# Optimization experiments

Measured on AMD Instinct MI355X. Metric: run time of the kernel, lower is better.

The kernel has to match this reference:

```python
import jax, jax.numpy as jnp
from jax import lax
import numpy as np

B, N_WAY, K_SHOT, Q, IMG = 8, 5, 1, 15, 84
D = 3      # repnet spatial output for imgsz=84
CF = 64    # repnet channels
C2 = CF + 2

def _conv(x, w, b):
    y = lax.conv_general_dilated(x, w, (1, 1), 'VALID', dimension_numbers=('NCHW', 'OIHW', 'NCHW'))
    return y + b[None, :, None, None]

def _maxpool2(x):
    return lax.reduce_window(x, -jnp.inf, lax.max, (1, 1, 2, 2), (1, 1, 2, 2), 'VALID')

def _avgpool5(x):
    return lax.reduce_window(x, 0.0, lax.add, (1, 1, 5, 5), (1, 1, 5, 5), 'VALID') / 25.0

def _bn(x, g, b):
    # train-mode BatchNorm2d: batch statistics over (N, H, W), biased variance, eps=1e-5
    m = jnp.mean(x, (0, 2, 3), keepdims=True)
    v = jnp.var(x, (0, 2, 3), keepdims=True)
    return (x - m) * lax.rsqrt(v + 1e-5) * g[None, :, None, None] + b[None, :, None, None]

def _repnet(x, cw1, cb1, bg1, bb1, cw2, cb2, bg2, bb2, cw3, cb3, bg3, bb3, cw4, cb4, bg4, bb4):
    x = jax.nn.relu(_bn(_maxpool2(_conv(x, cw1, cb1)), bg1, bb1))
    x = jax.nn.relu(_bn(_maxpool2(_conv(x, cw2, cb2)), bg2, bb2))
    x = jax.nn.relu(_bn(_conv(x, cw3, cb3), bg3, bb3))
    x = jax.nn.relu(_bn(_conv(x, cw4, cb4), bg4, bb4))
    return _avgpool5(x)

def _forward(support_x, support_y, query_x, query_y, cw1, cb1, bg1, bb1, cw2, cb2, bg2, bb2, cw3, cb3, bg3, bb3, cw4, cb4, bg4, bb4, gW1, gb1, gW2, gb2, gW3, gb3, gW4, gb4, fW1, fb1, fW2, fb2, fW3, fb3, fW4, fb4):
    b, setsz = support_x.shape[:2]
    q = query_x.shape[1]
    rep = lambda z: _repnet(z, cw1, cb1, bg1, bb1, cw2, cb2, bg2, bb2, cw3, cb3, bg3, bb3, cw4, cb4, bg4, bb4)
    sup = rep(support_x.reshape(b * setsz, 3, IMG, IMG)).reshape(b, setsz, CF, D, D)
    qry = rep(query_x.reshape(b * q, 3, IMG, IMG)).reshape(b, q, CF, D, D)
    sup = sup.reshape(b, N_WAY, K_SHOT, CF, D, D).sum(2)  # sum over shots -> (b, n_way, c, d, d)
    setsz = N_WAY
    sy = support_y[:, ::K_SHOT]
    ii, jj = jnp.meshgrid(jnp.arange(D), jnp.arange(D), indexing='ij')
    coord = jnp.stack([ii, jj]).astype(jnp.float32) / D  # (2, d, d): ch0 = i/d, ch1 = j/d
    sup = jnp.concatenate([sup, jnp.broadcast_to(coord, (b, setsz, 2, D, D))], axis=2)  # (b,s,66,d,d)
    qry = jnp.concatenate([qry, jnp.broadcast_to(coord, (b, q, 2, D, D))], axis=2)      # (b,q,66,d,d)
    d2 = D * D
    sup = sup.reshape(b, setsz, C2, d2)
    qry = qry.reshape(b, q, C2, d2)
    # pair feature is cat([support_feat, query_feat]); split g's first layer so the
    # (b,q,s,d2,d2,2c) pair tensor is never materialized: g1([s;q]) = s@Ws + q@Wq + b1
    Ws, Wq = gW1[:C2], gW1[C2:]
    A = jnp.einsum('bscp,ck->bspk', sup, Ws)   # (b, s, d2, 256)
    Bq = jnp.einsum('bqcp,ck->bqpk', qry, Wq)  # (b, q, d2, 256)
    h = jax.nn.relu(A[:, None, :, :, None, :] + Bq[:, :, None, None, :, :] + gb1)  # (b,q,s,d2,d2,256)
    h = jax.nn.relu(h @ gW2 + gb2)
    h = jax.nn.relu(h @ gW3 + gb3)
    h = jax.nn.relu(h @ gW4 + gb4)
    x_f = h.sum((3, 4))  # sum over all d2*d2 pixel pairs -> (b, q, s, 256)
    h = jax.nn.relu(x_f @ fW1 + fb1)
    h = jax.nn.relu(h @ fW2 + fb2)  # nn.Dropout treated as identity (deterministic reference)
    h = jax.nn.relu(h @ fW3 + fb3)
    o = h @ fW4 + fb4  # (b, q, s, 64)
    score = jnp.sqrt(jnp.sum(o * o, axis=-1))  # L2 norm over feature dim -> (b, q, s)
    n = jnp.sqrt(jnp.sum(score * score, axis=2, keepdims=True))
    score = score / n * (n * n / (1.0 + n * n))  # squash
    ap = sy[:, None, :] == query_y[:, :, None]  # exactly one True per (b, q)
    an = ~ap
    score_ap = jnp.sum(jnp.where(ap, score, 0.0), axis=2, keepdims=True)
    MARGIN = 0.2
    loss = jnp.sum(jax.nn.relu(score - score_ap + MARGIN) * an)
    return loss

def setup_inputs() -> dict:
    key = jax.random.key(0)
    ks = iter(jax.random.split(key, 48))
    nrm = lambda shape, s: jax.random.normal(next(ks), shape, jnp.float32) * s
    inp = {}
    inp['support_x'] = nrm((B, N_WAY * K_SHOT, 3, IMG, IMG), 1.0)
    inp['support_y'] = jnp.tile(jnp.arange(N_WAY, dtype=jnp.int32), (B, 1))
    inp['query_x'] = nrm((B, Q, 3, IMG, IMG), 1.0)
    inp['query_y'] = jax.random.randint(next(ks), (B, Q), 0, N_WAY, dtype=jnp.int32)
    inp['cw1'] = nrm((64, 3, 3, 3), 0.19); inp['cb1'] = nrm((64,), 0.02)
    inp['bg1'] = 1.0 + nrm((64,), 0.05); inp['bb1'] = nrm((64,), 0.02)
    inp['cw2'] = nrm((64, 64, 3, 3), 0.042); inp['cb2'] = nrm((64,), 0.02)
    inp['bg2'] = 1.0 + nrm((64,), 0.05); inp['bb2'] = nrm((64,), 0.02)
    inp['cw3'] = nrm((64, 64, 3, 3), 0.042); inp['cb3'] = nrm((64,), 0.02)
    inp['bg3'] = 1.0 + nrm((64,), 0.05); inp['bb3'] = nrm((64,), 0.02)
    inp['cw4'] = nrm((64, 64, 3, 3), 0.042); inp['cb4'] = nrm((64,), 0.02)
    inp['bg4'] = 1.0 + nrm((64,), 0.05); inp['bb4'] = nrm((64,), 0.02)
    inp['gW1'] = nrm((2 * C2, 256), 0.087); inp['gb1'] = nrm((256,), 0.02)
    inp['gW2'] = nrm((256, 256), 0.0625); inp['gb2'] = nrm((256,), 0.02)
    inp['gW3'] = nrm((256, 256), 0.0625); inp['gb3'] = nrm((256,), 0.02)
    inp['gW4'] = nrm((256, 256), 0.0625); inp['gb4'] = nrm((256,), 0.02)
    inp['fW1'] = nrm((256, 256), 0.0625); inp['fb1'] = nrm((256,), 0.02)
    inp['fW2'] = nrm((256, 256), 0.0625); inp['fb2'] = nrm((256,), 0.02)
    inp['fW3'] = nrm((256, 128), 0.0625); inp['fb3'] = nrm((128,), 0.02)
    inp['fW4'] = nrm((128, 64), 0.088); inp['fb4'] = nrm((64,), 0.02)
    return inp

def reference(support_x, support_y, query_x, query_y, cw1, cb1, bg1, bb1, cw2, cb2, bg2, bb2, cw3, cb3, bg3, bb3, cw4, cb4, bg4, bb4, gW1, gb1, gW2, gb2, gW3, gb3, gW4, gb4, fW1, fb1, fW2, fb2, fW3, fb3, fW4, fb4):
    return _forward(support_x, support_y, query_x, query_y, cw1, cb1, bg1, bb1, cw2, cb2, bg2, bb2, cw3, cb3, bg3, bb3, cw4, cb4, bg4, bb4, gW1, gb1, gW2, gb2, gW3, gb3, gW4, gb4, fW1, fb1, fW2, fb2, fW3, fb3, fW4, fb4)
```

## Files before the change

### kernel.cpp

```cpp
#include <hip/hip_runtime.h>
#include <hip/hip_bf16.h>

typedef __hip_bfloat16 bf16;
typedef __attribute__((ext_vector_type(8))) short short8;
typedef __attribute__((ext_vector_type(4))) short bfx4;
typedef __attribute__((ext_vector_type(4))) float f32x4;

#define DEV __device__ __forceinline__

static constexpr int NSUP = 40;
static constexpr int NQRY = 120;
static constexpr int NIMG = 160;
static constexpr int GM   = 48600;
static constexpr int GMP  = 48640;
static constexpr int NBS  = 128;
static constexpr int NBQ  = 384;

DEV float b2f(short s) {
    union { unsigned int u; float f; } v; v.u = ((unsigned int)(unsigned short)s) << 16; return v.f;
}
DEV short bfbits(float v) {
    bf16 h = __float2bfloat16(v);
    union { bf16 b; short s; } u; u.b = h; return u.s;
}

#define GLL(gp, lp) __builtin_amdgcn_global_load_lds( \
    (const __attribute__((address_space(1))) void*)(gp), \
    (__attribute__((address_space(3))) void*)(lp), 16, 0, 0)

__global__ void nhwc4_kernel(const float* sx, const float* qx, bf16* img) {
    int idx = blockIdx.x * 256 + threadIdx.x;
    if (idx >= NIMG * 7056) return;
    int n = idx / 7056, p = idx % 7056;
    const float* im = ((n < NSUP) ? sx + (size_t)n * 3 * 7056 : qx + (size_t)(n - NSUP) * 3 * 7056) + p;
    bfx4 o;
    o[0] = bfbits(im[0]);
    o[1] = bfbits(im[7056]);
    o[2] = bfbits(im[14112]);
    o[3] = 0;
    *(bfx4*)&img[(size_t)idx * 4] = o;
}

__global__ void wc1m_kernel(const float* cw1, bf16* Wc1) {
    int idx = blockIdx.x * 256 + threadIdx.x;
    if (idx >= 4096) return;
    int oc = idx >> 6, k = idx & 63;
    int ky = k >> 4, r = k & 15;
    float v = 0.f;
    if (ky < 3 && r < 12) {
        int kx = r >> 2, ic = r & 3;
        if (ic < 3) v = cw1[oc * 27 + ic * 9 + ky * 3 + kx];
    }
    Wc1[idx] = __float2bfloat16(v);
}

__global__ __launch_bounds__(256) void conv1m_kernel(
        const bf16* __restrict__ img, const bf16* __restrict__ Wc1,
        const float* __restrict__ cb1, bf16* __restrict__ out) {
    int n = blockIdx.x;
    int wv = threadIdx.x >> 6, ln = threadIdx.x & 63;
    int pr = ln & 15, kg = ln >> 4;
    int t0 = (blockIdx.y * 4 + wv) * 16;
    int t = t0 + pr;
    int tc = t < 1681 ? t : 1680;
    int pyt = tc / 41, pxt = tc % 41;
    const bf16* ib = img + (size_t)n * 28224;

    short8 wf[4][2];
    #pragma unroll
    for (int mt = 0; mt < 4; ++mt)
        #pragma unroll
        for (int h = 0; h < 2; ++h)
            wf[mt][h] = *(const short8*)&Wc1[(size_t)(mt * 16 + pr) * 64 + h * 32 + kg * 8];

    int r8 = (kg & 1) * 8;
    int kyb = kg >> 1;
    short8 pf[4][2];
    #pragma unroll
    for (int nt = 0; nt < 4; ++nt) {
        int py = 2 * pyt + (nt >> 1), px = 2 * pxt + (nt & 1);
        #pragma unroll
        for (int h = 0; h < 2; ++h) {
            int ky = h * 2 + kyb;
            short8 f = {0, 0, 0, 0, 0, 0, 0, 0};
            if (ky < 3) {
                const bf16* p = ib + ((py + ky) * 84 + px) * 4 + r8;
                if (r8 == 0) {
                    bfx4 a0 = *(const bfx4*)p, a1 = *(const bfx4*)(p + 4);
                    f[0] = a0[0]; f[1] = a0[1]; f[2] = a0[2]; f[3] = a0[3];
                    f[4] = a1[0]; f[5] = a1[1]; f[6] = a1[2]; f[7] = a1[3];
                } else {
                    bfx4 a0 = *(const bfx4*)p;
                    f[0] = a0[0]; f[1] = a0[1]; f[2] = a0[2]; f[3] = a0[3];
                }
            }
            pf[nt][h] = f;
        }
    }

    f32x4 acc[4][4];
    #pragma unroll
    for (int a = 0; a < 4; ++a)
        #pragma unroll
        for (int b = 0; b < 4; ++b)
            #pragma unroll
            for (int r = 0; r < 4; ++r) acc[a][b][r] = 0.f;

    #pragma unroll
    for (int h = 0; h < 2; ++h)
        #pragma unroll
        for (int mt = 0; mt < 4; ++mt)
            #pragma unroll
            for (int nt = 0; nt < 4; ++nt)
                acc[mt][nt] = __builtin_amdgcn_mfma_f32_16x16x32_bf16(
                    wf[mt][h], pf[nt][h], acc[mt][nt], 0, 0, 0);

    if (t < 1681) {
        bf16* ob = out + ((size_t)n * 1681 + t) * 64;
        #pragma unroll
        for (int mt = 0; mt < 4; ++mt) {
            f32x4 v = acc[mt][0];
            #pragma unroll
            for (int nt = 1; nt < 4; ++nt)
                #pragma unroll
                for (int r = 0; r < 4; ++r) v[r] = fmaxf(v[r], acc[mt][nt][r]);
            bfx4 o;
            #pragma unroll
            for (int r = 0; r < 4; ++r) o[r] = bfbits(v[r] + cb1[mt * 16 + kg * 4 + r]);
            *(bfx4*)&ob[mt * 16 + kg * 4] = o;
        }
    }
}

__global__ void wtp_kernel(const float* cw2, const float* cw3, const float* cw4, bf16* Wp) {
    int idx = blockIdx.x * 256 + threadIdx.x;
    if (idx >= 3 * 64 * 584) return;
    int L = idx / (64 * 584), r = idx % (64 * 584);
    int oc = r / 584, kk = r % 584;
    const float* src = (L == 0) ? cw2 : (L == 1) ? cw3 : cw4;
    float v = 0.f;
    if (kk < 576) {
        int ic = kk & 63, tap = kk >> 6;
        v = src[oc * 576 + ic * 9 + tap];
    }
    Wp[idx] = __float2bfloat16(v);
}

__global__ void wtg_kernel(const float* gW2, const float* gW3, const float* gW4, bf16* WTg) {
    int idx = blockIdx.x * 256 + threadIdx.x;
    if (idx >= 3 * 65536) return;
    int L = idx >> 16, r = idx & 65535, n = r >> 8, k = r & 255;
    const float* W = (L == 0) ? gW2 : (L == 1) ? gW3 : gW4;
    WTg[idx] = __float2bfloat16(W[k * 256 + n]);
}

__global__ void stats_nhwc_kernel(const bf16* buf, int HW, float* partial) {
    int blk = blockIdx.x;
    bool qg = blk >= NBS;
    int b0 = qg ? blk - NBS : blk;
    int nb = qg ? NBQ : NBS;
    const bf16* base = buf + (qg ? (size_t)NSUP * HW * 64 : 0);
    long rows = (long)(qg ? NQRY : NSUP) * HW;
    int tid = threadIdx.x;
    int sub = tid & 7, rl = tid >> 3;
    float s1[8], s2[8];
    #pragma unroll
    for (int j = 0; j < 8; ++j) { s1[j] = 0.f; s2[j] = 0.f; }
    for (long r = (long)b0 * 32 + rl; r < rows; r += (long)nb * 32) {
        short8 v = *(const short8*)&base[r * 64 + sub * 8];
        #pragma unroll
        for (int j = 0; j < 8; ++j) { float f = b2f(v[j]); s1[j] += f; s2[j] += f * f; }
    }
    __shared__ float l1[256][8], l2[256][8];
    #pragma unroll
    for (int j = 0; j < 8; ++j) { l1[tid][j] = s1[j]; l2[tid][j] = s2[j]; }
    __syncthreads();
    if (tid < 64) {
        int su = tid >> 3, j = tid & 7;
        float a = 0.f, b = 0.f;
        for (int k = 0; k < 32; ++k) { a += l1[su + k * 8][j]; b += l2[su + k * 8][j]; }
        partial[blk * 128 + tid] = a;
        partial[blk * 128 + 64 + tid] = b;
    }
}

__global__ __launch_bounds__(1024) void bnfin_kernel(
        const float* partial, const float* gam, const float* bet,
        int HW, float* scsh) {
    int tid = threadIdx.x;
    int out = tid >> 3;
    int part = tid & 7;
    int g = out >> 6, c = out & 63;
    int b0 = g ? NBS : 0, nb = g ? NBQ : NBS;
    float s1 = 0.f, s2 = 0.f;
    for (int b = b0 + part; b < b0 + nb; b += 8) {
        s1 += partial[b * 128 + c];
        s2 += partial[b * 128 + 64 + c];
    }
    __shared__ float r1[1024], r2[1024];
    r1[tid] = s1; r2[tid] = s2;
    __syncthreads();
    if (part == 0) {
        #pragma unroll
        for (int j = 1; j < 8; ++j) { s1 += r1[tid + j]; s2 += r2[tid + j]; }
        float cnt = (float)((g ? NQRY : NSUP)) * (float)HW;
        float mean = s1 / cnt;
        float var = s2 / cnt - mean * mean;
        float istd = rsqrtf(var + 1e-5f);
        float sc = gam[c] * istd;
        scsh[out] = sc;
        scsh[128 + out] = bet[c] - mean * sc;
    }
}

__global__ void bnrelu_nhwc_kernel(bf16* buf, const float* scsh, int HW, int total8) {
    int idx = blockIdx.x * 256 + threadIdx.x;
    if (idx >= total8) return;
    size_t e0 = (size_t)idx * 8;
    int c0 = (int)(e0 & 63);
    int g = (int)(e0 / ((size_t)HW * 64)) >= NSUP ? 1 : 0;
    short8 v = *(short8*)&buf[e0];
    short8 o;
    #pragma unroll
    for (int j = 0; j < 8; ++j) {
        int c = c0 + j;
        float f = b2f(v[j]) * scsh[g * 64 + c] + scsh[128 + g * 64 + c];
        o[j] = bfbits(fmaxf(f, 0.f));
    }
    *(short8*)&buf[e0] = o;
}

template <int IW, int OW, bool POOL, int NT>
__global__ __launch_bounds__(256) void convmfma_kernel(
        const bf16* __restrict__ in, const bf16* __restrict__ Wp,
        const float* __restrict__ cb, bf16* __restrict__ out) {
    constexpr int M  = OW * OW;
    constexpr int PW = OW / 2;
    constexpr int MP = POOL ? PW * PW : M;
    constexpr int T  = NIMG * MP;
    constexpr int NPF = POOL ? 4 : NT;

    int wv = threadIdx.x >> 6, ln = threadIdx.x & 63;
    int pr = ln & 15, kg = ln >> 4;

    const bf16* pptr[NPF];
    int pxv[NPF];
    if (POOL) {
        int gp = (blockIdx.x * 4 + wv) * 16 + pr;
        int gpc = gp < T ? gp : T - 1;
        pxv[0] = gp;
        int n = gpc / MP, pp = gpc % MP;
        int py = pp / PW, px = pp % PW;
        const bf16* ib = in + (size_t)n * (IW * IW * 64) + kg * 8;
        #pragma unroll
        for (int nt = 0; nt < 4; ++nt)
            pptr[nt] = ib + ((2 * py + (nt >> 1)) * IW + 2 * px + (nt & 1)) * 64;
    } else {
        #pragma unroll
        for (int nt = 0; nt < NT; ++nt) {
            int gp = (blockIdx.x * 4 + wv) * (16 * NT) + nt * 16 + pr;
            int gpc = gp < T ? gp : T - 1;
            pxv[nt] = gp;
            int n = gpc / M, pix = gpc % M;
            int y = pix / OW, x = pix % OW;
            pptr[nt] = in + ((size_t)n * (IW * IW) + y * IW + x) * 64 + kg * 8;
        }
    }
    const bf16* wb = Wp + kg * 8;

    f32x4 acc[4][NPF];
    #pragma unroll
    for (int a = 0; a < 4; ++a)
        #pragma unroll
        for (int b = 0; b < NPF; ++b)
            #pragma unroll
            for (int r = 0; r < 4; ++r) acc[a][b][r] = 0.f;

    #pragma unroll
    for (int tap = 0; tap < 9; ++tap) {
        int off0 = ((tap / 3) * IW + (tap % 3)) * 64;
        #pragma unroll
        for (int h = 0; h < 2; ++h) {
            int off = off0 + h * 32;
            int wk = (tap * 2 + h) * 32;
            short8 wf[4], pf[NPF];
            #pragma unroll
            for (int mt = 0; mt < 4; ++mt)
                wf[mt] = *(const short8*)(wb + (size_t)(mt * 16 + pr) * 584 + wk);
            #pragma unroll
            for (int nt = 0; nt < NPF; ++nt)
                pf[nt] = *(const short8*)(pptr[nt] + off);
            #pragma unroll
            for (int mt = 0; mt < 4; ++mt)
                #pragma unroll
                for (int nt = 0; nt < NPF; ++nt)
                    acc[mt][nt] = __builtin_amdgcn_mfma_f32_16x16x32_bf16(
                        wf[mt], pf[nt], acc[mt][nt], 0, 0, 0);
        }
    }

    if (POOL) {
        int gp = pxv[0];
        if (gp < T) {
            bf16* ob = out + (size_t)gp * 64;
            #pragma unroll
            for (int mt = 0; mt < 4; ++mt) {
                f32x4 v = acc[mt][0];
                #pragma unroll
                for (int nt = 1; nt < 4; ++nt)
                    #pragma unroll
                    for (int r = 0; r < 4; ++r) v[r] = fmaxf(v[r], acc[mt][nt][r]);
                bfx4 o;
                #pragma unroll
                for (int r = 0; r < 4; ++r) o[r] = bfbits(v[r] + cb[mt * 16 + kg * 4 + r]);
                *(bfx4*)&ob[mt * 16 + kg * 4] = o;
            }
        }
    } else {
        #pragma unroll
        for (int mt = 0; mt < 4; ++mt) {
            float bv[4];
            #pragma unroll
            for (int r = 0; r < 4; ++r) bv[r] = cb[mt * 16 + kg * 4 + r];
            #pragma unroll
            for (int nt = 0; nt < NPF; ++nt) {
                if (pxv[nt] < T) {
                    bfx4 o;
                    #pragma unroll
                    for (int r = 0; r < 4; ++r) o[r] = bfbits(acc[mt][nt][r] + bv[r]);
                    *(bfx4*)&out[(size_t)pxv[nt] * 64 + mt * 16 + kg * 4] = o;
                }
            }
        }
    }
}

__global__ void bnpool_kernel(const bf16* buf4, const float* scsh, float* feat) {
    int wid = blockIdx.x * 4 + (threadIdx.x >> 6);
    int c = threadIdx.x & 63;
    if (wid >= 1440) return;
    int n = wid / 9, p9 = wid % 9;
    int g = n >= NSUP;
    float sc = scsh[g * 64 + c], sh = scsh[128 + g * 64 + c];
    int ii = p9 / 3, jj = p9 % 3;
    const bf16* base = buf4 + ((size_t)n * 225 + ii * 5 * 15 + jj * 5) * 64 + c;
    float s = 0;
    #pragma unroll
    for (int u = 0; u < 5; ++u)
        #pragma unroll
        for (int v = 0; v < 5; ++v)
            s += fmaxf(__bfloat162float(base[(u * 15 + v) * 64]) * sc + sh, 0.f);
    feat[n * 576 + c * 9 + p9] = s * 0.04f;
}

__global__ void proj_kernel(const float* feat, const float* gW1, float* A, float* Bq) {
    int n = blockIdx.x, k = threadIdx.x;
    const float* W = (n < NSUP) ? gW1 : gW1 + 66 * 256;
    float* out = (n < NSUP) ? A + (size_t)n * 9 * 256 : Bq + (size_t)(n - NSUP) * 9 * 256;
    const float* fb = feat + n * 576;
    for (int p = 0; p < 9; ++p) {
        float acc = 0;
        for (int c = 0; c < 64; ++c) acc += fb[c * 9 + p] * W[c * 256 + k];
        acc += ((float)(p / 3) * (1.f / 3.f)) * W[64 * 256 + k];
        acc += ((float)(p % 3) * (1.f / 3.f)) * W[65 * 256 + k];
        out[p * 256 + k] = acc;
    }
}

__global__ void h0_kernel(const float* A, const float* Bq, const float* gb1, bf16* H) {
    int tid = threadIdx.x;
    int row = blockIdx.x * 8 + (tid >> 5);
    int col = (tid & 31) * 8;
    short8 o;
    if (row < GM) {
        int bqs = row / 81, r81 = row % 81;
        int ps = r81 / 9, pq = r81 % 9;
        int b = bqs / 75, r75 = bqs % 75, q = r75 / 5, s = r75 % 5;
        const float* Ar = A + ((size_t)((b * 5 + s) * 9 + ps)) * 256 + col;
        const float* Br = Bq + ((size_t)((b * 15 + q) * 9 + pq)) * 256 + col;
        #pragma unroll
        for (int j = 0; j < 8; ++j) {
            float v = Ar[j] + Br[j] + gb1[col + j];
            o[j] = bfbits(fmaxf(v, 0.f));
        }
    } else {
        #pragma unroll
        for (int j = 0; j < 8; ++j) o[j] = 0;
    }
    *(short8*)&H[(size_t)row * 256 + col] = o;
}

__global__ __launch_bounds__(256) void gemm_relu_kernel(
        const bf16* __restrict__ Ain, const bf16* __restrict__ WT,
        const float* __restrict__ bias, bf16* __restrict__ out) {
    __shared__ __align__(16) short As[2][4096];
    __shared__ __align__(16) short Bs[2][4096];
    int bm0 = blockIdx.x * 128;
    int bn0 = blockIdx.y * 128;
    int tid = threadIdx.x, wv = tid >> 6, ln = tid & 63;
    int wm = wv >> 1, wn = wv & 1;

    int srow = (wv * 2) * 16 + (ln >> 2);
    int scol = (ln & 3) * 8;
    const bf16* Ag = Ain + (size_t)(bm0 + srow) * 256 + scol;
    const bf16* Bg = WT + (size_t)(bn0 + srow) * 256 + scol;

    f32x4 acc[4][4];
    #pragma unroll
    for (int m = 0; m < 4; ++m)
        #pragma unroll
        for (int n = 0; n < 4; ++n)
            #pragma unroll
            for (int r = 0; r < 4; ++r) acc[m][n][r] = 0.f;

    int ar = (wm * 64 + (ln & 15)) * 32 + (ln >> 4) * 8;
    int br = (wn * 64 + (ln & 15)) * 32 + (ln >> 4) * 8;

    GLL(Ag,            &As[0][(wv * 2) * 512]);
    GLL(Ag + 16 * 256, &As[0][(wv * 2 + 1) * 512]);
    GLL(Bg,            &Bs[0][(wv * 2) * 512]);
    GLL(Bg + 16 * 256, &Bs[0][(wv * 2 + 1) * 512]);
    __syncthreads();

    int cur = 0;
    for (int kt = 0; kt < 8; ++kt) {
        if (kt < 7) {
            int k0 = (kt + 1) * 32;
            GLL(Ag + k0,            &As[cur ^ 1][(wv * 2) * 512]);
            GLL(Ag + 16 * 256 + k0, &As[cur ^ 1][(wv * 2 + 1) * 512]);
            GLL(Bg + k0,            &Bs[cur ^ 1][(wv * 2) * 512]);
            GLL(Bg + 16 * 256 + k0, &Bs[cur ^ 1][(wv * 2 + 1) * 512]);
        }
        short8 a[4], b[4];
        #pragma unroll
        for (int m = 0; m < 4; ++m) a[m] = *(const short8*)&As[cur][ar + m * 512];
        #pragma unroll
        for (int n = 0; n < 4; ++n) b[n] = *(const short8*)&Bs[cur][br + n * 512];
        #pragma unroll
        for (int m = 0; m < 4; ++m)
            #pragma unroll
            for (int n = 0; n < 4; ++n)
                acc[m][n] = __builtin_amdgcn_mfma_f32_16x16x32_bf16(a[m], b[n], acc[m][n], 0, 0, 0);
        __syncthreads();
        cur ^= 1;
    }

    int orow = bm0 + wm * 64 + (ln >> 4) * 4;
    int ocol = bn0 + wn * 64 + (ln & 15);
    #pragma unroll
    for (int n = 0; n < 4; ++n) {
        float bv = bias[ocol + n * 16];
        #pragma unroll
        for (int m = 0; m < 4; ++m) {
            #pragma unroll
            for (int r = 0; r < 4; ++r) {
                float v = acc[m][n][r] + bv;
                out[(size_t)(orow + m * 16 + r) * 256 + ocol + n * 16] =
                    __float2bfloat16(fmaxf(v, 0.f));
            }
        }
    }
}

__global__ void xfred_kernel(const bf16* H, float* xf) {
    int bqs = blockIdx.x, t = threadIdx.x;
    const bf16* p = H + (size_t)bqs * 81 * 256 + t;
    float s = 0;
    for (int r = 0; r < 81; ++r) s += __bfloat162float(p[r * 256]);
    xf[(size_t)bqs * 256 + t] = s;
}

__global__ void fchain_kernel(const float* xf, const float* fW1, const float* fb1,
                              const float* fW2, const float* fb2,
                              const float* fW3, const float* fb3,
                              const float* fW4, const float* fb4,
                              const int* sy, const int* qy, float* lossp) {
    __shared__ float xb[5 * 257];
    __shared__ float ob[5 * 64];
    __shared__ float scs[8];
    int bid = blockIdx.x;
    int b = bid / 15, q = bid % 15;
    int tid = threadIdx.x;
    for (int s = 0; s < 5; ++s) xb[s * 257 + tid] = xf[((size_t)(b * 15 + q) * 5 + s) * 256 + tid];
    __syncthreads();
    #pragma unroll
    for (int L = 0; L < 2; ++L) {
        const float* W = (L == 0) ? fW1 : fW2;
        const float* bias = (L == 0) ? fb1 : fb2;
        float acc[5];
        #pragma unroll
        for (int s = 0; s < 5; ++s) acc[s] = bias[tid];
        for (int ki = 0; ki < 256; ++ki) {
            float w = W[ki * 256 + tid];
            #pragma unroll
            for (int s = 0; s < 5; ++s) acc[s] += xb[s * 257 + ki] * w;
        }
        __syncthreads();
        #pragma unroll
        for (int s = 0; s < 5; ++s) xb[s * 257 + tid] = fmaxf(acc[s], 0.f);
        __syncthreads();
    }
    {
        float acc[5];
        if (tid < 128) {
            #pragma unroll
            for (int s = 0; s < 5; ++s) acc[s] = fb3[tid];
            for (int ki = 0; ki < 256; ++ki) {
                float w = fW3[ki * 128 + tid];
                #pragma unroll
                for (int s = 0; s < 5; ++s) acc[s] += xb[s * 257 + ki] * w;
            }
        }
        __syncthreads();
        if (tid < 128) {
            #pragma unroll
            for (int s = 0; s < 5; ++s) xb[s * 257 + tid] = fmaxf(acc[s], 0.f);
        }
        __syncthreads();
    }
    {
        if (tid < 64) {
            float acc[5];
            #pragma unroll
            for (int s = 0; s < 5; ++s) acc[s] = fb4[tid];
            for (int ki = 0; ki < 128; ++ki) {
                float w = fW4[ki * 64 + tid];
                #pragma unroll
                for (int s = 0; s < 5; ++s) acc[s] += xb[s * 257 + ki] * w;
            }
            #pragma unroll
            for (int s = 0; s < 5; ++s) ob[s * 64 + tid] = acc[s];
        }
        __syncthreads();
    }
    if (tid < 5) {
        float t = 0;
        for (int k = 0; k < 64; ++k) { float v = ob[tid * 64 + k]; t += v * v; }
        scs[tid] = sqrtf(t);
    }
    __syncthreads();
    if (tid == 0) {
        float n2 = 0;
        for (int s = 0; s < 5; ++s) n2 += scs[s] * scs[s];
        float n = sqrtf(n2);
        float f = n / (1.f + n2);
        int qyv = qy[b * 15 + q];
        float sc[5]; bool ap[5]; float sap = 0;
        for (int s = 0; s < 5; ++s) {
            sc[s] = scs[s] * f;
            ap[s] = (sy[b * 5 + s] == qyv);
            if (ap[s]) sap += sc[s];
        }
        float lp = 0;
        for (int s = 0; s < 5; ++s)
            if (!ap[s]) lp += fmaxf(sc[s] - sap + 0.2f, 0.f);
        lossp[bid] = lp;
    }
}

__global__ void lreduce_kernel(const float* lossp, float* out) {
    __shared__ float r[128];
    int tid = threadIdx.x;
    r[tid] = (tid < NQRY) ? lossp[tid] : 0.f;
    __syncthreads();
    for (int off = 64; off; off >>= 1) {
        if (tid < off) r[tid] += r[tid + off];
        __syncthreads();
    }
    if (tid == 0) out[0] = r[0];
}

extern "C" void kernel_launch(void* const* d_in, const int* in_sizes, int n_in,
                              void* d_out, int out_size, void* d_ws, size_t ws_size,
                              hipStream_t stream) {
    const float* sx  = (const float*)d_in[0];
    const int*   syp = (const int*)d_in[1];
    const float* qx  = (const float*)d_in[2];
    const int*   qyp = (const int*)d_in[3];
    const float* cw1 = (const float*)d_in[4];  const float* cb1 = (const float*)d_in[5];
    const float* bg1 = (const float*)d_in[6];  const float* bb1 = (const float*)d_in[7];
    const float* cw2 = (const float*)d_in[8];  const float* cb2 = (const float*)d_in[9];
    const float* bg2 = (const float*)d_in[10]; const float* bb2 = (const float*)d_in[11];
    const float* cw3 = (const float*)d_in[12]; const float* cb3 = (const float*)d_in[13];
    const float* bg3 = (const float*)d_in[14]; const float* bb3 = (const float*)d_in[15];
    const float* cw4 = (const float*)d_in[16]; const float* cb4 = (const float*)d_in[17];
    const float* bg4 = (const float*)d_in[18]; const float* bb4 = (const float*)d_in[19];
    const float* gW1 = (const float*)d_in[20]; const float* gb1 = (const float*)d_in[21];
    const float* gW2 = (const float*)d_in[22]; const float* gb2 = (const float*)d_in[23];
    const float* gW3 = (const float*)d_in[24]; const float* gb3 = (const float*)d_in[25];
    const float* gW4 = (const float*)d_in[26]; const float* gb4 = (const float*)d_in[27];
    const float* fW1 = (const float*)d_in[28]; const float* fb1 = (const float*)d_in[29];
    const float* fW2 = (const float*)d_in[30]; const float* fb2 = (const float*)d_in[31];
    const float* fW3 = (const float*)d_in[32]; const float* fb3 = (const float*)d_in[33];
    const float* fW4 = (const float*)d_in[34]; const float* fb4 = (const float*)d_in[35];

    char* w = (char*)d_ws;
    size_t off = 0;
    bf16*  buf1  = (bf16*)(w + off); off += 34426880ull;
    bf16*  hbuf  = (bf16*)(w + off); off += 31150080ull;
    bf16*  pbuf2 = (bf16*)(w + off); off += 7393280ull;
    bf16*  buf3  = (bf16*)(w + off); off += 5918720ull;
    bf16*  buf4  = (bf16*)(w + off); off += 4608000ull;
    float* feat  = (float*)(w + off); off += 368640ull;
    float* Abuf  = (float*)(w + off); off += 368640ull;
    float* Bbuf  = (float*)(w + off); off += 1105920ull;
    float* xf    = (float*)(w + off); off += 614400ull;
    float* partial = (float*)(w + off); off += 262144ull;
    float* scsh  = (float*)(w + off); off += 4096ull;
    bf16*  imgN  = (bf16*)(w + off); off += 9031680ull;
    bf16*  Wc1   = (bf16*)(w + off); off += 8192ull;
    bf16*  Wp    = (bf16*)(w + off); off += 224256ull;
    bf16*  WTg   = (bf16*)(w + off); off += 393216ull;
    float* lossp = (float*)(w + off); off += 512ull;

    float* scsh1 = scsh;        float* scsh2 = scsh + 256;
    float* scsh3 = scsh + 512;  float* scsh4 = scsh + 768;
    bf16* Wp2 = Wp;
    bf16* Wp3 = Wp + 64 * 584;
    bf16* Wp4 = Wp + 2 * 64 * 584;

    bf16* Hb0 = buf1;
    bf16* Hb1 = hbuf;

    nhwc4_kernel<<<(NIMG * 7056 + 255) / 256, 256, 0, stream>>>(sx, qx, imgN);
    wc1m_kernel<<<16, 256, 0, stream>>>(cw1, Wc1);
    wtp_kernel<<<(3 * 64 * 584 + 255) / 256, 256, 0, stream>>>(cw2, cw3, cw4, Wp);
    wtg_kernel<<<(3 * 65536 + 255) / 256, 256, 0, stream>>>(gW2, gW3, gW4, WTg);

    conv1m_kernel<<<dim3(NIMG, 27), 256, 0, stream>>>(imgN, Wc1, cb1, buf1);
    stats_nhwc_kernel<<<NBS + NBQ, 256, 0, stream>>>(buf1, 1681, partial);
    bnfin_kernel<<<1, 1024, 0, stream>>>(partial, bg1, bb1, 1681, scsh1);
    bnrelu_nhwc_kernel<<<(2151680 + 255) / 256, 256, 0, stream>>>(buf1, scsh1, 1681, 2151680);

    convmfma_kernel<41, 39, true, 4><<<dim3(903), 256, 0, stream>>>(buf1, Wp2, cb2, pbuf2);
    stats_nhwc_kernel<<<NBS + NBQ, 256, 0, stream>>>(pbuf2, 361, partial);
    bnfin_kernel<<<1, 1024, 0, stream>>>(partial, bg2, bb2, 361, scsh2);
    bnrelu_nhwc_kernel<<<(462080 + 255) / 256, 256, 0, stream>>>(pbuf2, scsh2, 361, 462080);

    convmfma_kernel<19, 17, false, 2><<<dim3(362), 256, 0, stream>>>(pbuf2, Wp3, cb3, buf3);
    stats_nhwc_kernel<<<NBS + NBQ, 256, 0, stream>>>(buf3, 289, partial);
    bnfin_kernel<<<1, 1024, 0, stream>>>(partial, bg3, bb3, 289, scsh3);
    bnrelu_nhwc_kernel<<<(369920 + 255) / 256, 256, 0, stream>>>(buf3, scsh3, 289, 369920);

    convmfma_kernel<17, 15, false, 2><<<dim3(282), 256, 0, stream>>>(buf3, Wp4, cb4, buf4);
    stats_nhwc_kernel<<<NBS + NBQ, 256, 0, stream>>>(buf4, 225, partial);
    bnfin_kernel<<<1, 1024, 0, stream>>>(partial, bg4, bb4, 225, scsh4);
    bnpool_kernel<<<360, 256, 0, stream>>>(buf4, scsh4, feat);

    proj_kernel<<<NIMG, 256, 0, stream>>>(feat, gW1, Abuf, Bbuf);

    h0_kernel<<<GMP / 8, 256, 0, stream>>>(Abuf, Bbuf, gb1, Hb0);
    dim3 ggrid(GMP / 128, 2);
    gemm_relu_kernel<<<ggrid, 256, 0, stream>>>(Hb0, WTg,          gb2, Hb1);
    gemm_relu_kernel<<<ggrid, 256, 0, stream>>>(Hb1, WTg + 65536,  gb3, Hb0);
    gemm_relu_kernel<<<ggrid, 256, 0, stream>>>(Hb0, WTg + 131072, gb4, Hb1);
    xfred_kernel<<<600, 256, 0, stream>>>(Hb1, xf);

    fchain_kernel<<<NQRY, 256, 0, stream>>>(xf, fW1, fb1, fW2, fb2, fW3, fb3, fW4, fb4,
                                            syp, qyp, lossp);

    lreduce_kernel<<<1, 128, 0, stream>>>(lossp, (float*)d_out);
}
```

Baseline: 372.2 us.

## Replace scalar fp32 f-MLP chain with bf16 MFMA GEMM kernels

The per-query fchain kernel, which ran four fp32 scalar matmul layers per block, is replaced by four launches of a tiled bf16 MFMA GEMM over all 600 rows (padded to 640), followed by a small score kernel that does the norms with wave shuffles. A new prep kernel transposes and pads the f-network weights to bf16 and zero-pads the last layer to 128 outputs. The aim is to move this chain onto the matrix cores and stop each block re-reading the weights from global memory. In exchange it adds four more kernel launches, stores intermediate activations in bf16 (lower precision), and launches only a few blocks per GEMM, so little of the GPU is busy.

```diff
diff --git a/kernel.cpp b/kernel.cpp
--- a/kernel.cpp
+++ b/kernel.cpp
@@ -154,6 +154,28 @@
     WTg[idx] = __float2bfloat16(W[k * 256 + n]);
 }
 
+__global__ void wtf_kernel(const float* fW1, const float* fW2, const float* fW3,
+                           const float* fW4, const float* fb4, bf16* fWT, float* fb4p) {
+    int idx = blockIdx.x * 256 + threadIdx.x;
+    if (idx < 65536) {
+        int n = idx >> 8, k = idx & 255;
+        fWT[idx] = __float2bfloat16(fW1[k * 256 + n]);
+    } else if (idx < 131072) {
+        int r = idx - 65536, n = r >> 8, k = r & 255;
+        fWT[idx] = __float2bfloat16(fW2[k * 256 + n]);
+    } else if (idx < 163840) {
+        int r = idx - 131072, n = r >> 8, k = r & 255;
+        fWT[idx] = __float2bfloat16(fW3[k * 128 + n]);
+    } else if (idx < 180224) {
+        int r = idx - 163840, n = r >> 7, k = r & 127;
+        float v = (n < 64) ? fW4[k * 64 + n] : 0.f;
+        fWT[idx] = __float2bfloat16(v);
+    } else if (idx < 180352) {
+        int i = idx - 180224;
+        fb4p[i] = (i < 64) ? fb4[i] : 0.f;
+    }
+}
+
 __global__ void stats_nhwc_kernel(const bf16* buf, int HW, float* partial) {
     int blk = blockIdx.x;
     bool qg = blk >= NBS;
@@ -462,98 +484,119 @@
     }
 }
 
-__global__ void xfred_kernel(const bf16* H, float* xf) {
+template <int KT, bool RELU, bool F32OUT>
+__global__ __launch_bounds__(256) void gemm_f_kernel(
+        const bf16* __restrict__ Ain, const bf16* __restrict__ WT,
+        const float* __restrict__ bias, void* __restrict__ outv, int ldo) {
+    constexpr int K = KT * 32;
+    __shared__ __align__(16) short As[2][4096];
+    __shared__ __align__(16) short Bs[2][4096];
+    int bm0 = blockIdx.x * 128;
+    int bn0 = blockIdx.y * 128;
+    int tid = threadIdx.x, wv = tid >> 6, ln = tid & 63;
+    int wm = wv >> 1, wn = wv & 1;
+
+    int srow = (wv * 2) * 16 + (ln >> 2);
+    int scol = (ln & 3) * 8;
+    const bf16* Ag = Ain + (size_t)(bm0 + srow) * K + scol;
+    const bf16* Bg = WT + (size_t)(bn0 + srow) * K + scol;
+
+    f32x4 acc[4][4];
+    #pragma unroll
+    for (int m = 0; m < 4; ++m)
+        #pragma unroll
+        for (int n = 0; n < 4; ++n)
+            #pragma unroll
+            for (int r = 0; r < 4; ++r) acc[m][n][r] = 0.f;
+
+    int ar = (wm * 64 + (ln & 15)) * 32 + (ln >> 4) * 8;
+    int br = (wn * 64 + (ln & 15)) * 32 + (ln >> 4) * 8;
+
+    GLL(Ag,          &As[0][(wv * 2) * 512]);
+    GLL(Ag + 16 * K, &As[0][(wv * 2 + 1) * 512]);
+    GLL(Bg,          &Bs[0][(wv * 2) * 512]);
+    GLL(Bg + 16 * K, &Bs[0][(wv * 2 + 1) * 512]);
+    __syncthreads();
+
+    int cur = 0;
+    for (int kt = 0; kt < KT; ++kt) {
+        if (kt < KT - 1) {
+            int k0 = (kt + 1) * 32;
+            GLL(Ag + k0,          &As[cur ^ 1][(wv * 2) * 512]);
+            GLL(Ag + 16 * K + k0, &As[cur ^ 1][(wv * 2 + 1) * 512]);
+            GLL(Bg + k0,          &Bs[cur ^ 1][(wv * 2) * 512]);
+            GLL(Bg + 16 * K + k0, &Bs[cur ^ 1][(wv * 2 + 1) * 512]);
+        }
+        short8 a[4], b[4];
+        #pragma unroll
+        for (int m = 0; m < 4; ++m) a[m] = *(const short8*)&As[cur][ar + m * 512];
+        #pragma unroll
+        for (int n = 0; n < 4; ++n) b[n] = *(const short8*)&Bs[cur][br + n * 512];
+        #pragma unroll
+        for (int m = 0; m < 4; ++m)
+            #pragma unroll
+            for (int n = 0; n < 4; ++n)
+                acc[m][n] = __builtin_amdgcn_mfma_f32_16x16x32_bf16(a[m], b[n], acc[m][n], 0, 0, 0);
+        __syncthreads();
+        cur ^= 1;
+    }
+
+    int orow = bm0 + wm * 64 + (ln >> 4) * 4;
+    int ocol = bn0 + wn * 64 + (ln & 15);
+    #pragma unroll
+    for (int n = 0; n < 4; ++n) {
+        float bv = bias[ocol + n * 16];
+        #pragma unroll
+        for (int m = 0; m < 4; ++m) {
+            #pragma unroll
+            for (int r = 0; r < 4; ++r) {
+                float v = acc[m][n][r] + bv;
+                if (RELU) v = fmaxf(v, 0.f);
+                size_t oi = (size_t)(orow + m * 16 + r) * ldo + ocol + n * 16;
+                if (F32OUT) ((float*)outv)[oi] = v;
+                else        ((bf16*)outv)[oi] = __float2bfloat16(v);
+            }
+        }
+    }
+}
+
+__global__ void xfred_kernel(const bf16* H, bf16* xfb) {
     int bqs = blockIdx.x, t = threadIdx.x;
-    const bf16* p = H + (size_t)bqs * 81 * 256 + t;
     float s = 0;
-    for (int r = 0; r < 81; ++r) s += __bfloat162float(p[r * 256]);
-    xf[(size_t)bqs * 256 + t] = s;
-}
-
-__global__ void fchain_kernel(const float* xf, const float* fW1, const float* fb1,
-                              const float* fW2, const float* fb2,
-                              const float* fW3, const float* fb3,
-                              const float* fW4, const float* fb4,
-                              const int* sy, const int* qy, float* lossp) {
-    __shared__ float xb[5 * 257];
-    __shared__ float ob[5 * 64];
+    if (bqs < 600) {
+        const bf16* p = H + (size_t)bqs * 81 * 256 + t;
+        for (int r = 0; r < 81; ++r) s += __bfloat162float(p[r * 256]);
+    }
+    xfb[(size_t)bqs * 256 + t] = __float2bfloat16(s);
+}
+
+__global__ void score_kernel(const float* F4, const int* sy, const int* qy, float* lossp) {
     __shared__ float scs[8];
     int bid = blockIdx.x;
-    int b = bid / 15, q = bid % 15;
     int tid = threadIdx.x;
-    for (int s = 0; s < 5; ++s) xb[s * 257 + tid] = xf[((size_t)(b * 15 + q) * 5 + s) * 256 + tid];
-    __syncthreads();
-    #pragma unroll
-    for (int L = 0; L < 2; ++L) {
-        const float* W = (L == 0) ? fW1 : fW2;
-        const float* bias = (L == 0) ? fb1 : fb2;
-        float acc[5];
-        #pragma unroll
-        for (int s = 0; s < 5; ++s) acc[s] = bias[tid];
-        for (int ki = 0; ki < 256; ++ki) {
-            float w = W[ki * 256 + tid];
-            #pragma unroll
-            for (int s = 0; s < 5; ++s) acc[s] += xb[s * 257 + ki] * w;
-        }
-        __syncthreads();
-        #pragma unroll
-        for (int s = 0; s < 5; ++s) xb[s * 257 + tid] = fmaxf(acc[s], 0.f);
-        __syncthreads();
-    }
-    {
-        float acc[5];
-        if (tid < 128) {
-            #pragma unroll
-            for (int s = 0; s < 5; ++s) acc[s] = fb3[tid];
-            for (int ki = 0; ki < 256; ++ki) {
-                float w = fW3[ki * 128 + tid];
-                #pragma unroll
-                for (int s = 0; s < 5; ++s) acc[s] += xb[s * 257 + ki] * w;
-            }
-        }
-        __syncthreads();
-        if (tid < 128) {
-            #pragma unroll
-            for (int s = 0; s < 5; ++s) xb[s * 257 + tid] = fmaxf(acc[s], 0.f);
-        }
-        __syncthreads();
-    }
-    {
-        if (tid < 64) {
-            float acc[5];
-            #pragma unroll
-            for (int s = 0; s < 5; ++s) acc[s] = fb4[tid];
-            for (int ki = 0; ki < 128; ++ki) {
-                float w = fW4[ki * 64 + tid];
-                #pragma unroll
-                for (int s = 0; s < 5; ++s) acc[s] += xb[s * 257 + ki] * w;
-            }
-            #pragma unroll
-            for (int s = 0; s < 5; ++s) ob[s * 64 + tid] = acc[s];
-        }
-        __syncthreads();
-    }
-    if (tid < 5) {
-        float t = 0;
-        for (int k = 0; k < 64; ++k) { float v = ob[tid * 64 + k]; t += v * v; }
-        scs[tid] = sqrtf(t);
-    }
+    int s = tid >> 6, k = tid & 63;
+    float v = F4[(size_t)(bid * 5 + s) * 128 + k];
+    float sum = v * v;
+    #pragma unroll
+    for (int m = 1; m < 64; m <<= 1) sum += __shfl_xor(sum, m);
+    if (k == 0) scs[s] = sqrtf(sum);
     __syncthreads();
     if (tid == 0) {
+        int b = bid / 15, q = bid % 15;
         float n2 = 0;
-        for (int s = 0; s < 5; ++s) n2 += scs[s] * scs[s];
+        for (int j = 0; j < 5; ++j) n2 += scs[j] * scs[j];
         float n = sqrtf(n2);
         float f = n / (1.f + n2);
         int qyv = qy[b * 15 + q];
         float sc[5]; bool ap[5]; float sap = 0;
-        for (int s = 0; s < 5; ++s) {
-            sc[s] = scs[s] * f;
-            ap[s] = (sy[b * 5 + s] == qyv);
-            if (ap[s]) sap += sc[s];
+        for (int j = 0; j < 5; ++j) {
+            sc[j] = scs[j] * f;
+            ap[j] = (sy[b * 5 + j] == qyv);
+            if (ap[j]) sap += sc[j];
         }
         float lp = 0;
-        for (int s = 0; s < 5; ++s)
-            if (!ap[s]) lp += fmaxf(sc[s] - sap + 0.2f, 0.f);
+        for (int j = 0; j < 5; ++j)
+            if (!ap[j]) lp += fmaxf(sc[j] - sap + 0.2f, 0.f);
         lossp[bid] = lp;
     }
 }
@@ -604,13 +647,19 @@
     float* feat  = (float*)(w + off); off += 368640ull;
     float* Abuf  = (float*)(w + off); off += 368640ull;
     float* Bbuf  = (float*)(w + off); off += 1105920ull;
-    float* xf    = (float*)(w + off); off += 614400ull;
+    bf16*  xfb   = (bf16*)(w + off); off += 327680ull;
+    bf16*  F1    = (bf16*)(w + off); off += 327680ull;
+    bf16*  F2    = (bf16*)(w + off); off += 327680ull;
+    bf16*  F3    = (bf16*)(w + off); off += 163840ull;
+    float* F4    = (float*)(w + off); off += 327680ull;
     float* partial = (float*)(w + off); off += 262144ull;
     float* scsh  = (float*)(w + off); off += 4096ull;
     bf16*  imgN  = (bf16*)(w + off); off += 9031680ull;
     bf16*  Wc1   = (bf16*)(w + off); off += 8192ull;
     bf16*  Wp    = (bf16*)(w + off); off += 224256ull;
     bf16*  WTg   = (bf16*)(w + off); off += 393216ull;
+    bf16*  fWT   = (bf16*)(w + off); off += 360448ull;
+    float* fb4p  = (float*)(w + off); off += 512ull;
     float* lossp = (float*)(w + off); off += 512ull;
 
     float* scsh1 = scsh;        float* scsh2 = scsh + 256;
@@ -618,6 +667,10 @@
     bf16* Wp2 = Wp;
     bf16* Wp3 = Wp + 64 * 584;
     bf16* Wp4 = Wp + 2 * 64 * 584;
+    bf16* fWT1 = fWT;
+    bf16* fWT2 = fWT + 65536;
+    bf16* fWT3 = fWT + 131072;
+    bf16* fWT4 = fWT + 163840;
 
     bf16* Hb0 = buf1;
     bf16* Hb1 = hbuf;
@@ -626,6 +679,7 @@
     wc1m_kernel<<<16, 256, 0, stream>>>(cw1, Wc1);
     wtp_kernel<<<(3 * 64 * 584 + 255) / 256, 256, 0, stream>>>(cw2, cw3, cw4, Wp);
     wtg_kernel<<<(3 * 65536 + 255) / 256, 256, 0, stream>>>(gW2, gW3, gW4, WTg);
+    wtf_kernel<<<(180352 + 255) / 256, 256, 0, stream>>>(fW1, fW2, fW3, fW4, fb4, fWT, fb4p);
 
     conv1m_kernel<<<dim3(NIMG, 27), 256, 0, stream>>>(imgN, Wc1, cb1, buf1);
     stats_nhwc_kernel<<<NBS + NBQ, 256, 0, stream>>>(buf1, 1681, partial);
@@ -654,10 +708,13 @@
     gemm_relu_kernel<<<ggrid, 256, 0, stream>>>(Hb0, WTg,          gb2, Hb1);
     gemm_relu_kernel<<<ggrid, 256, 0, stream>>>(Hb1, WTg + 65536,  gb3, Hb0);
     gemm_relu_kernel<<<ggrid, 256, 0, stream>>>(Hb0, WTg + 131072, gb4, Hb1);
-    xfred_kernel<<<600, 256, 0, stream>>>(Hb1, xf);
-
-    fchain_kernel<<<NQRY, 256, 0, stream>>>(xf, fW1, fb1, fW2, fb2, fW3, fb3, fW4, fb4,
-                                            syp, qyp, lossp);
-
+    xfred_kernel<<<640, 256, 0, stream>>>(Hb1, xfb);
+
+    gemm_f_kernel<8, true,  false><<<dim3(5, 2), 256, 0, stream>>>(xfb, fWT1, fb1,  (void*)F1, 256);
+    gemm_f_kernel<8, true,  false><<<dim3(5, 2), 256, 0, stream>>>(F1,  fWT2, fb2,  (void*)F2, 256);
+    gemm_f_kernel<8, true,  false><<<dim3(5, 1), 256, 0, stream>>>(F2,  fWT3, fb3,  (void*)F3, 128);
+    gemm_f_kernel<4, false, true ><<<dim3(5, 1), 256, 0, stream>>>(F3,  fWT4, fb4p, (void*)F4, 128);
+
+    score_kernel<<<NQRY, 320, 0, stream>>>(F4, syp, qyp, lossp);
     lreduce_kernel<<<1, 128, 0, stream>>>(lossp, (float*)d_out);
 }
```

Result: faster. 363.9 us (-2.2%).
